# Performance work log

Hardware: AMD Instinct MI355X
Metric: run time of the kernel (lower is better)

The kernel has to match this reference:

```python
import jax, jax.numpy as jnp
import numpy as np

B = 16384
NEG = 10
V = 100000
E = 128

def setup_inputs() -> dict:
    key = jax.random.key(0)
    k1, k2, k3, k4, k5 = jax.random.split(key, 5)
    input_word = jax.random.randint(k1, (B,), 0, V)
    context_word = jax.random.randint(k2, (B,), 0, V)
    noise_words = jax.random.randint(k3, (B * NEG,), 0, V)
    # torch init: uniform_(-1, 1)
    W_in = jax.random.uniform(k4, (V, E), jnp.float32, -1.0, 1.0)
    W_ctx = jax.random.uniform(k5, (V, E), jnp.float32, -1.0, 1.0)
    return {"input_word": input_word, "context_word": context_word,
            "noise_words": noise_words, "W_in": W_in, "W_ctx": W_ctx}

def reference(input_word, context_word, noise_words, W_in, W_ctx):
    center = W_in[input_word]               # [B, E]
    ctx = W_ctx[context_word]               # [B, E]
    # positive score: per-example dot product
    out_loss = jax.nn.log_sigmoid(jnp.einsum('be,be->b', ctx, center))  # [B]
    noise = W_ctx[noise_words].reshape(B, NEG, E)                       # [B, NEG, E]
    # negative scores: -u_k . v_c
    neg_scores = -jnp.einsum('bke,be->bk', noise, center)               # [B, NEG]
    noise_loss = jax.nn.log_sigmoid(neg_scores).sum(axis=1)             # [B]
    return -(out_loss + noise_loss).mean()
```

## Files before the change

kernel.cpp:

```cpp
#include <hip/hip_runtime.h>
#include <hip/hip_bf16.h>

constexpr int kB   = 16384;
constexpr int kNeg = 10;
constexpr int kE   = 128;
constexpr int kWavesPerBlock = 4;
constexpr int kExPerWave     = 4;
constexpr int kBlocks = kB / (kWavesPerBlock * kExPerWave);

__device__ __forceinline__ float log_sigmoid(float x) {
    return fminf(x, 0.0f) - log1pf(expf(-fabsf(x)));
}

__device__ __forceinline__ float dot4(float4 a, float4 b) {
    return a.x * b.x + a.y * b.y + a.z * b.z + a.w * b.w;
}

__global__ __launch_bounds__(256, 4) void w2v_loss_kernel(
    const int*   __restrict__ input_word,
    const int*   __restrict__ context_word,
    const int*   __restrict__ noise_words,
    const float* __restrict__ W_in,
    const float* __restrict__ W_ctx,
    float*       __restrict__ partials)
{
    const int lane = threadIdx.x & 63;
    const int wave = threadIdx.x >> 6;
    const int l16  = lane & 15;
    const int slot = lane >> 4;

    const int wave_global = blockIdx.x * kWavesPerBlock + wave;
    const int b = wave_global * kExPerWave + slot;

    const int iw = input_word[b];
    const int cw = context_word[b];
    const float4* __restrict__ crow = (const float4*)(W_in  + (size_t)iw * kE);
    const float4* __restrict__ xrow = (const float4*)(W_ctx + (size_t)cw * kE);
    const float4 c0 = crow[l16];
    const float4 c1 = crow[l16 + 16];
    const float4 x0 = xrow[l16];
    const float4 x1 = xrow[l16 + 16];
    float pos = dot4(c0, x0) + dot4(c1, x1);

    float negp[kNeg];
    #pragma unroll
    for (int k = 0; k < kNeg; ++k) {
        const int nw = noise_words[b * kNeg + k];
        const float4* __restrict__ nrow = (const float4*)(W_ctx + (size_t)nw * kE);
        const float4 n0 = nrow[l16];
        const float4 n1 = nrow[l16 + 16];
        negp[k] = dot4(c0, n0) + dot4(c1, n1);
    }

    #pragma unroll
    for (int off = 8; off > 0; off >>= 1) {
        pos += __shfl_xor(pos, off);
        #pragma unroll
        for (int k = 0; k < kNeg; ++k)
            negp[k] += __shfl_xor(negp[k], off);
    }

    float v = pos;
    #pragma unroll
    for (int k = 0; k < kNeg; ++k)
        v = (l16 == k + 1) ? -negp[k] : v;
    float s = (l16 < 1 + kNeg) ? log_sigmoid(v) : 0.0f;

    #pragma unroll
    for (int off = 8; off > 0; off >>= 1)
        s += __shfl_xor(s, off);
    s += __shfl_xor(s, 16);
    s += __shfl_xor(s, 32);

    __shared__ float smem[kWavesPerBlock];
    if (lane == 0) smem[wave] = s;
    __syncthreads();
    if (threadIdx.x == 0)
        partials[blockIdx.x] = smem[0] + smem[1] + smem[2] + smem[3];
}

__global__ __launch_bounds__(256) void w2v_reduce_kernel(
    const float* __restrict__ partials,
    float*       __restrict__ out)
{
    float acc = 0.0f;
    for (int i = threadIdx.x; i < kBlocks; i += 256)
        acc += partials[i];

    #pragma unroll
    for (int off = 32; off > 0; off >>= 1)
        acc += __shfl_xor(acc, off);

    __shared__ float smem[4];
    const int lane = threadIdx.x & 63;
    const int wave = threadIdx.x >> 6;
    if (lane == 0) smem[wave] = acc;
    __syncthreads();
    if (threadIdx.x == 0) {
        const float total = smem[0] + smem[1] + smem[2] + smem[3];
        out[0] = -total / (float)kB;
    }
}

extern "C" void kernel_launch(void* const* d_in, const int* in_sizes, int n_in,
                              void* d_out, int out_size, void* d_ws, size_t ws_size,
                              hipStream_t stream) {
    const int*   input_word   = (const int*)d_in[0];
    const int*   context_word = (const int*)d_in[1];
    const int*   noise_words  = (const int*)d_in[2];
    const float* W_in         = (const float*)d_in[3];
    const float* W_ctx        = (const float*)d_in[4];
    float*       out          = (float*)d_out;
    float*       partials     = (float*)d_ws;

    w2v_loss_kernel<<<kBlocks, 256, 0, stream>>>(
        input_word, context_word, noise_words, W_in, W_ctx, partials);
    w2v_reduce_kernel<<<1, 256, 0, stream>>>(partials, out);
}
```

Baseline: 125.3 us.

## Map each example to 32 lanes with one float4 per row and batched gathers

Each example is now handled by half a wave, so every lane loads a single float4 per row instead of two. Grid size doubles to 2048 blocks. All noise indices and noise rows are fetched up front before any compute, which puts more memory requests in flight per lane. In exchange, shuffle reductions gain one extra step, total shuffle work per example grows, and more registers are live at once.

```diff
diff --git a/kernel.cpp b/kernel.cpp
--- a/kernel.cpp
+++ b/kernel.cpp
@@ -5,7 +5,7 @@
 constexpr int kNeg = 10;
 constexpr int kE   = 128;
 constexpr int kWavesPerBlock = 4;
-constexpr int kExPerWave     = 4;
+constexpr int kExPerWave     = 2;
 constexpr int kBlocks = kB / (kWavesPerBlock * kExPerWave);
 
 __device__ __forceinline__ float log_sigmoid(float x) {
@@ -26,34 +26,33 @@
 {
     const int lane = threadIdx.x & 63;
     const int wave = threadIdx.x >> 6;
-    const int l16  = lane & 15;
-    const int slot = lane >> 4;
+    const int half = lane >> 5;
+    const int l32  = lane & 31;
 
-    const int wave_global = blockIdx.x * kWavesPerBlock + wave;
-    const int b = wave_global * kExPerWave + slot;
+    const int b = (blockIdx.x * kWavesPerBlock + wave) * kExPerWave + half;
 
     const int iw = input_word[b];
     const int cw = context_word[b];
-    const float4* __restrict__ crow = (const float4*)(W_in  + (size_t)iw * kE);
-    const float4* __restrict__ xrow = (const float4*)(W_ctx + (size_t)cw * kE);
-    const float4 c0 = crow[l16];
-    const float4 c1 = crow[l16 + 16];
-    const float4 x0 = xrow[l16];
-    const float4 x1 = xrow[l16 + 16];
-    float pos = dot4(c0, x0) + dot4(c1, x1);
+    int nw[kNeg];
+    #pragma unroll
+    for (int k = 0; k < kNeg; ++k)
+        nw[k] = noise_words[b * kNeg + k];
 
+    const float4 c = ((const float4*)(W_in  + (size_t)iw * kE))[l32];
+    const float4 x = ((const float4*)(W_ctx + (size_t)cw * kE))[l32];
+    float4 nv[kNeg];
+    #pragma unroll
+    for (int k = 0; k < kNeg; ++k)
+        nv[k] = ((const float4*)(W_ctx + (size_t)nw[k] * kE))[l32];
+
+    float pos = dot4(c, x);
     float negp[kNeg];
     #pragma unroll
-    for (int k = 0; k < kNeg; ++k) {
-        const int nw = noise_words[b * kNeg + k];
-        const float4* __restrict__ nrow = (const float4*)(W_ctx + (size_t)nw * kE);
-        const float4 n0 = nrow[l16];
-        const float4 n1 = nrow[l16 + 16];
-        negp[k] = dot4(c0, n0) + dot4(c1, n1);
-    }
+    for (int k = 0; k < kNeg; ++k)
+        negp[k] = dot4(c, nv[k]);
 
     #pragma unroll
-    for (int off = 8; off > 0; off >>= 1) {
+    for (int off = 16; off > 0; off >>= 1) {
         pos += __shfl_xor(pos, off);
         #pragma unroll
         for (int k = 0; k < kNeg; ++k)
@@ -63,13 +62,12 @@
     float v = pos;
     #pragma unroll
     for (int k = 0; k < kNeg; ++k)
-        v = (l16 == k + 1) ? -negp[k] : v;
-    float s = (l16 < 1 + kNeg) ? log_sigmoid(v) : 0.0f;
+        v = (l32 == k + 1) ? -negp[k] : v;
+    float s = (l32 < 1 + kNeg) ? log_sigmoid(v) : 0.0f;
 
     #pragma unroll
-    for (int off = 8; off > 0; off >>= 1)
+    for (int off = 16; off > 0; off >>= 1)
         s += __shfl_xor(s, off);
-    s += __shfl_xor(s, 16);
     s += __shfl_xor(s, 32);
 
     __shared__ float smem[kWavesPerBlock];
```

Result: no change. 124.7 us (-0.5%).
